# Kernel tuning notes

Hardware: AMD Instinct MI355X
Metric: run time of the kernel (lower is better)

The kernel has to match this reference:

```python
import jax, jax.numpy as jnp
import numpy as np

EPS = 1e-4
HEADS = 8
DIM_HEAD = 32
BALANCE = 0.3


def _normalize(x, dims):
    # torch normalize(): norm over `dims` in fp32; norm = eps + norm*sqrt(norm.numel()/x.numel())
    red = 1
    for d in dims:
        red *= x.shape[d]
    norm = jnp.sqrt(jnp.sum(jnp.square(x.astype(jnp.float32)), axis=dims, keepdims=True))
    norm = EPS + norm / np.sqrt(red)
    return x / norm.astype(x.dtype)


def _mpconv1x1(x, w, gain=1.0):
    # MPConv forward (eval mode): weight-normalize per output channel, scale, 1x1 conv
    w = w.astype(jnp.float32)
    w = _normalize(w, (1, 2, 3))
    fan_in = w.shape[1] * w.shape[2] * w.shape[3]
    w = (w * (gain / np.sqrt(fan_in))).astype(x.dtype)[:, :, 0, 0]  # [out, in]
    return jnp.einsum('oi,nihw->nohw', w, x)


def setup_inputs() -> dict:
    key = jax.random.key(0)
    k1, k2, k3 = jax.random.split(key, 3)
    x = jax.random.normal(k1, (2, 256, 48, 48), dtype=jnp.float32)
    w_qkv = jax.random.normal(k2, (768, 256, 1, 1), dtype=jnp.float32)
    w_out = jax.random.normal(k3, (256, 256, 1, 1), dtype=jnp.float32)
    return {"x": x, "w_qkv": w_qkv, "w_out": w_out}


def reference(x, w_qkv, w_out):
    n, c, h, w_sp = x.shape
    seq = h * w_sp
    y = _mpconv1x1(x, w_qkv)                          # [n, 3c, h, w]
    y = y.reshape(n, HEADS, DIM_HEAD, 3, seq)         # channel split: head x dim_head x 3
    y = _normalize(y, (2,))                           # L2-normalize over dim_head axis
    q = y[:, :, :, 0, :]
    k = y[:, :, :, 1, :]
    v = y[:, :, :, 2, :]
    # scores [n, h, q, k] with k scaled by 1/sqrt(dim_head)
    att = jax.nn.softmax(jnp.einsum('nhcq,nhck->nhqk', q, k) / np.sqrt(DIM_HEAD), axis=3)
    y = jnp.einsum('nhqk,nhck->nhcq', att, v)         # [n, heads, dim_head, seq]
    y = _mpconv1x1(y.reshape(n, c, h, w_sp), w_out)
    t = BALANCE
    # mp_sum: lerp then magnitude-preserving rescale
    return (x + t * (y - x)) / np.sqrt((1 - t) ** 2 + t ** 2)
```

## Files before the change

### kernel.cpp

```cpp
#include <hip/hip_runtime.h>
#include <math.h>

#define EPSN 1e-4f
#define SEQ 2304

using bf16x8 = __attribute__((ext_vector_type(8))) short;
using f32x4  = __attribute__((ext_vector_type(4))) float;

__device__ inline unsigned short f2bf(float x) {
    union { float f; unsigned u; } c; c.f = x;
    unsigned u = c.u;
    u += 0x7fffu + ((u >> 16) & 1u);
    return (unsigned short)(u >> 16);
}

__device__ inline unsigned cvt_pk_bf16(float lo, float hi) {
    unsigned r;
    asm("v_cvt_pk_bf16_f32 %0, %1, %2" : "=v"(r) : "v"(lo), "v"(hi));
    return r;
}
__device__ inline void permlane32_swap(unsigned &a, unsigned &b) {
    asm("v_permlane32_swap_b32 %0, %1" : "+v"(a), "+v"(b));
}
__device__ inline void permlane16_swap(unsigned &a, unsigned &b) {
    asm("v_permlane16_swap_b32 %0, %1" : "+v"(a), "+v"(b));
}

__global__ __launch_bounds__(256) void prep_kernel(const float* __restrict__ w_qkv,
                                                   const float* __restrict__ w_out,
                                                   const float* __restrict__ x,
                                                   unsigned short* __restrict__ wqb,
                                                   unsigned short* __restrict__ wob,
                                                   unsigned short* __restrict__ xt) {
    __shared__ __align__(16) unsigned short T[16][72];
    int bid = blockIdx.x;
    if (bid < 256) {
        int wave = threadIdx.x >> 6, lane = threadIdx.x & 63;
        int row = bid * 4 + wave;
        const float* src;
        unsigned short* dst;
        if (row < 768) { src = w_qkv + (size_t)row * 256; dst = wqb + (size_t)row * 256; }
        else           { src = w_out + (size_t)(row - 768) * 256; dst = wob + (size_t)(row - 768) * 256; }
        float4 v = *(const float4*)&src[lane * 4];
        float ss = v.x * v.x + v.y * v.y + v.z * v.z + v.w * v.w;
        for (int off = 32; off > 0; off >>= 1) ss += __shfl_xor(ss, off, 64);
        float sc = 1.0f / (sqrtf(ss) + 16.0f * EPSN);
        unsigned p0 = (unsigned)f2bf(v.x * sc) | ((unsigned)f2bf(v.y * sc) << 16);
        unsigned p1 = (unsigned)f2bf(v.z * sc) | ((unsigned)f2bf(v.w * sc) << 16);
        *(uint2*)&dst[lane * 4] = make_uint2(p0, p1);
    } else {
        int e0 = bid - 256;
        int n = e0 / 576;
        int r = e0 % 576;
        int ct = r / 144;
        int r2 = r % 144;
        int st = r2 >> 2, sq = r2 & 3;
        int tid = threadIdx.x;
        int c = tid >> 2, sv = (tid & 3) * 4;
        float4 v = *(const float4*)&x[(size_t)(n * 256 + ct * 64 + c) * SEQ + st * 64 + sq * 16 + sv];
        T[sv + 0][c] = f2bf(v.x);
        T[sv + 1][c] = f2bf(v.y);
        T[sv + 2][c] = f2bf(v.z);
        T[sv + 3][c] = f2bf(v.w);
        __syncthreads();
        int s = tid >> 4, cb = (tid & 15) * 4;
        uint2 t2 = *(const uint2*)&T[s][cb];
        *(uint2*)&xt[(size_t)(n * SEQ + st * 64 + sq * 16 + s) * 256 + ct * 64 + cb] = t2;
    }
}

__global__ __launch_bounds__(256) void qkv_fused_kernel(const unsigned short* __restrict__ xt,
                                                        const unsigned short* __restrict__ wqb,
                                                        unsigned short* __restrict__ qn,
                                                        unsigned short* __restrict__ kn,
                                                        unsigned short* __restrict__ vn) {
    __shared__ float Cs[96][65];
    __shared__ __align__(16) unsigned short Vls[32][72];
    int bid = blockIdx.x;
    int xcd = bid & 7, j = bid >> 3;
    int h = j & 7;
    int tilej = xcd * 9 + (j >> 3);
    int st = tilej % 36, n = tilej / 36;
    int tid = threadIdx.x;
    int wave = tid >> 6, lane = tid & 63;
    int ln = lane & 15, quad = lane >> 4;
    const unsigned short* Abase = wqb + (size_t)(h * 96 + ln) * 256 + quad * 8;
    const unsigned short* Bbase = xt + (size_t)(n * SEQ + st * 64 + wave * 16 + ln) * 256 + quad * 8;
    f32x4 acc[6];
#pragma unroll
    for (int m = 0; m < 6; ++m) acc[m] = (f32x4){0.f, 0.f, 0.f, 0.f};
#pragma unroll
    for (int kc = 0; kc < 8; ++kc) {
        bf16x8 b = *(const bf16x8*)(Bbase + kc * 32);
#pragma unroll
        for (int m = 0; m < 6; ++m) {
            bf16x8 a = *(const bf16x8*)(Abase + (size_t)(m * 16) * 256 + kc * 32);
            acc[m] = __builtin_amdgcn_mfma_f32_16x16x32_bf16(a, b, acc[m], 0, 0, 0);
        }
    }
#pragma unroll
    for (int m = 0; m < 6; ++m)
#pragma unroll
        for (int r = 0; r < 4; ++r)
            Cs[m * 16 + quad * 4 + r][wave * 16 + ln] = acc[m][r];
    __syncthreads();
    int nh = n * 8 + h;
    if (tid < 192) {
        int sl = tid & 63, wh = tid >> 6;
        int s = st * 64 + sl;
        float v[32];
        float ss = 0.f;
#pragma unroll
        for (int d = 0; d < 32; ++d) { v[d] = Cs[3 * d + wh][sl]; ss += v[d] * v[d]; }
        float inv = 1.0f / (EPSN + sqrtf(ss * (1.0f / 32.0f)));
        if (wh == 0) inv *= 0.17677669529663687f * 1.4426950408889634f;
        if (wh == 2) {
#pragma unroll
            for (int d = 0; d < 32; ++d) Vls[d][sl] = f2bf(v[d] * inv);
        } else {
            unsigned short* dst = (wh == 1 ? kn : qn) + (size_t)nh * 73728 + (size_t)s * 32;
            unsigned wbuf[16];
#pragma unroll
            for (int j2 = 0; j2 < 16; ++j2)
                wbuf[j2] = (unsigned)f2bf(v[2 * j2] * inv) | ((unsigned)f2bf(v[2 * j2 + 1] * inv) << 16);
#pragma unroll
            for (int j2 = 0; j2 < 4; ++j2) {
                uint4 t4 = make_uint4(wbuf[4 * j2], wbuf[4 * j2 + 1], wbuf[4 * j2 + 2], wbuf[4 * j2 + 3]);
                *(uint4*)(dst + j2 * 8) = t4;
            }
        }
    }
    __syncthreads();
    {
        int d = tid >> 3, sj = (tid & 7) * 8;
        uint4 t4 = *(const uint4*)&Vls[d][sj];
        *(uint4*)&vn[(size_t)nh * 73728 + (size_t)d * SEQ + st * 64 + sj] = t4;
    }
}

__global__ __launch_bounds__(256) void attn_mfma_kernel(const unsigned short* __restrict__ qn,
                                                        const unsigned short* __restrict__ kn,
                                                        const unsigned short* __restrict__ vn,
                                                        float* __restrict__ Opart,
                                                        float* __restrict__ Lpart) {
    __shared__ __align__(16) unsigned short Ks[2][64][40];
    __shared__ __align__(16) unsigned short Vs[2][32][72];
    int tid = threadIdx.x;
    int wq = tid >> 6, lane = tid & 63;
    int ln = lane & 15, quad = lane >> 4;
    int bid = blockIdx.x;
    int xcd = bid & 7, bi = bid >> 3;
    int nh = xcd * 2 + (bi >= 72);
    int bi2 = (bi >= 72) ? bi - 72 : bi;
    int qt = bi2 % 36, kz = bi2 / 36;
    const unsigned short* Qg = qn + (size_t)nh * 73728;
    const unsigned short* Kg = kn + (size_t)nh * 73728;
    const unsigned short* Vg = vn + (size_t)nh * 73728;

    bf16x8 qf = *(const bf16x8*)(Qg + (size_t)(qt * 64 + wq * 16 + ln) * 32 + quad * 8);
    bf16x8 ones;
#pragma unroll
    for (int i = 0; i < 8; ++i) ones[i] = (short)0x3F80;

    f32x4 o0 = {0.f, 0.f, 0.f, 0.f};
    f32x4 o1 = {0.f, 0.f, 0.f, 0.f};
    f32x4 lac = {0.f, 0.f, 0.f, 0.f};

    int s0 = kz * 18 * 64;

    auto compute_tile = [&](int bsel) {
        const f32x4 zero = {0.f, 0.f, 0.f, 0.f};
        unsigned w[4][2];
#pragma unroll
        for (int c = 0; c < 4; ++c) {
            bf16x8 kf = *(const bf16x8*)(&Ks[bsel][c * 16 + ln][quad * 8]);
            f32x4 sc = __builtin_amdgcn_mfma_f32_16x16x32_bf16(kf, qf, zero, 0, 0, 0);
            w[c][0] = cvt_pk_bf16(exp2f(sc[0]), exp2f(sc[1]));
            w[c][1] = cvt_pk_bf16(exp2f(sc[2]), exp2f(sc[3]));
        }
#pragma unroll
        for (int kc = 0; kc < 2; ++kc) {
            unsigned a0 = w[2 * kc][0], b0 = w[2 * kc + 1][0];
            permlane32_swap(a0, b0);
            permlane16_swap(a0, b0);
            unsigned a1 = w[2 * kc][1], b1 = w[2 * kc + 1][1];
            permlane32_swap(a1, b1);
            permlane16_swap(a1, b1);
            union { unsigned u[4]; bf16x8 v8; } pk;
            pk.u[0] = a0; pk.u[1] = a1; pk.u[2] = b0; pk.u[3] = b1;
            bf16x8 v0 = *(const bf16x8*)(&Vs[bsel][ln][kc * 32 + quad * 8]);
            bf16x8 v1 = *(const bf16x8*)(&Vs[bsel][16 + ln][kc * 32 + quad * 8]);
            lac = __builtin_amdgcn_mfma_f32_16x16x32_bf16(pk.v8, ones, lac, 0, 0, 0);
            o0  = __builtin_amdgcn_mfma_f32_16x16x32_bf16(pk.v8, v0, o0, 0, 0, 0);
            o1  = __builtin_amdgcn_mfma_f32_16x16x32_bf16(pk.v8, v1, o1, 0, 0, 0);
        }
    };

    uint4 kA = *(const uint4*)(Kg + (size_t)s0 * 32 + tid * 8);
    uint4 vA = *(const uint4*)(Vg + (size_t)(tid >> 3) * SEQ + s0 + (tid & 7) * 8);
    *(uint4*)(&Ks[0][tid >> 2][(tid & 3) * 8]) = kA;
    *(uint4*)(&Vs[0][tid >> 3][(tid & 7) * 8]) = vA;
    uint4 kB = *(const uint4*)(Kg + (size_t)(s0 + 64) * 32 + tid * 8);
    uint4 vB = *(const uint4*)(Vg + (size_t)(tid >> 3) * SEQ + (s0 + 64) + (tid & 7) * 8);

    for (int i = 0; i < 18; i += 2) {
        if (i + 2 < 18) {
            int sn = s0 + (i + 2) * 64;
            kA = *(const uint4*)(Kg + (size_t)sn * 32 + tid * 8);
            vA = *(const uint4*)(Vg + (size_t)(tid >> 3) * SEQ + sn + (tid & 7) * 8);
        }
        __syncthreads();
        compute_tile(0);
        *(uint4*)(&Ks[1][tid >> 2][(tid & 3) * 8]) = kB;
        *(uint4*)(&Vs[1][tid >> 3][(tid & 7) * 8]) = vB;
        if (i + 3 < 18) {
            int sn = s0 + (i + 3) * 64;
            kB = *(const uint4*)(Kg + (size_t)sn * 32 + tid * 8);
            vB = *(const uint4*)(Vg + (size_t)(tid >> 3) * SEQ + sn + (tid & 7) * 8);
        }
        __syncthreads();
        compute_tile(1);
        if (i + 2 < 18) {
            *(uint4*)(&Ks[0][tid >> 2][(tid & 3) * 8]) = kA;
            *(uint4*)(&Vs[0][tid >> 3][(tid & 7) * 8]) = vA;
        }
    }

    float* Ob = Opart + ((size_t)(kz * 16 + nh) * 36 + qt) * 2048;
    float* Lb = Lpart + ((size_t)(kz * 16 + nh) * 36 + qt) * 64;
#pragma unroll
    for (int r = 0; r < 4; ++r) {
        int ql = wq * 16 + quad * 4 + r;
        Ob[ql * 32 + ln]      = o0[r];
        Ob[ql * 32 + 16 + ln] = o1[r];
        if (ln == 0) Lb[ql] = lac[r];
    }
}

__global__ __launch_bounds__(256) void attn_reduce_kernel(const float* __restrict__ Opart,
                                                          const float* __restrict__ Lpart,
                                                          unsigned short* __restrict__ y2t) {
    int qt = blockIdx.x, nh = blockIdx.y;
    int n = nh >> 3, h = nh & 7;
    size_t s0 = (size_t)nh * 36 + qt;
    const float* O0 = Opart + s0 * 2048;
    const float* O1 = Opart + (s0 + 16 * 36) * 2048;
    const float* L0 = Lpart + s0 * 64;
    const float* L1 = Lpart + (s0 + 16 * 36) * 64;
#pragma unroll
    for (int p = 0; p < 2; ++p) {
        int idx = (threadIdx.x + p * 256) * 4;
        int q = idx >> 5, c = idx & 31;
        float inv = 1.0f / (L0[q] + L1[q]);
        float4 a = *(const float4*)&O0[idx];
        float4 b = *(const float4*)&O1[idx];
        float r0 = (a.x + b.x) * inv;
        float r1 = (a.y + b.y) * inv;
        float r2 = (a.z + b.z) * inv;
        float r3 = (a.w + b.w) * inv;
        *(uint2*)&y2t[((size_t)(n * SEQ) + qt * 64 + q) * 256 + h * 32 + c] =
            make_uint2(cvt_pk_bf16(r0, r1), cvt_pk_bf16(r2, r3));
    }
}

__global__ __launch_bounds__(256) void out_gemm_kernel(const unsigned short* __restrict__ y2t,
                                                       const unsigned short* __restrict__ wob,
                                                       const float* __restrict__ x,
                                                       float* __restrict__ out) {
    int st = blockIdx.x;
    int mt = blockIdx.y;
    int n  = blockIdx.z;
    int tid = threadIdx.x;
    int wave = tid >> 6, lane = tid & 63;
    int ln = lane & 15, quad = lane >> 4;
    int m0 = mt * 64 + wave * 16;
    const unsigned short* Abase = wob + (size_t)(m0 + ln) * 256 + quad * 8;
    const unsigned short* Bbase = y2t + (size_t)(n * SEQ + st * 32 + ln) * 256 + quad * 8;
    f32x4 acc[2];
#pragma unroll
    for (int c = 0; c < 2; ++c) acc[c] = (f32x4){0.f, 0.f, 0.f, 0.f};
#pragma unroll
    for (int kc = 0; kc < 8; ++kc) {
        bf16x8 a = *(const bf16x8*)(Abase + kc * 32);
#pragma unroll
        for (int c = 0; c < 2; ++c) {
            bf16x8 b = *(const bf16x8*)(Bbase + (size_t)(c * 16) * 256 + kc * 32);
            acc[c] = __builtin_amdgcn_mfma_f32_16x16x32_bf16(a, b, acc[c], 0, 0, 0);
        }
    }
    const float c0f = 0.7f * 1.3130643285972254f;
    const float c1f = 0.3f * 1.3130643285972254f;
#pragma unroll
    for (int c = 0; c < 2; ++c)
#pragma unroll
        for (int r = 0; r < 4; ++r) {
            int o = m0 + quad * 4 + r;
            int s = st * 32 + c * 16 + ln;
            size_t idx = (size_t)(n * 256 + o) * SEQ + s;
            out[idx] = c0f * x[idx] + c1f * acc[c][r];
        }
}

extern "C" void kernel_launch(void* const* d_in, const int* in_sizes, int n_in,
                              void* d_out, int out_size, void* d_ws, size_t ws_size,
                              hipStream_t stream) {
    (void)in_sizes; (void)n_in; (void)out_size; (void)ws_size;
    const float* x     = (const float*)d_in[0];
    const float* w_qkv = (const float*)d_in[1];
    const float* w_out = (const float*)d_in[2];
    float* out = (float*)d_out;
    float* ws  = (float*)d_ws;
    unsigned short* wqb = (unsigned short*)(ws);
    unsigned short* wob = (unsigned short*)(ws + 98304);
    unsigned short* xt  = (unsigned short*)(ws + 131072);
    unsigned short* y2t = (unsigned short*)(ws + 131072);
    unsigned short* qn  = (unsigned short*)(ws + 720896);
    unsigned short* kn  = (unsigned short*)(ws + 1310720);
    unsigned short* vn  = (unsigned short*)(ws + 1900544);
    float* Opart = ws + 2490368;
    float* Lpart = ws + 4849664;

    hipLaunchKernelGGL(prep_kernel, dim3(1408), dim3(256), 0, stream,
                       w_qkv, w_out, x, wqb, wob, xt);
    hipLaunchKernelGGL(qkv_fused_kernel, dim3(576), dim3(256), 0, stream,
                       xt, wqb, qn, kn, vn);
    hipLaunchKernelGGL(attn_mfma_kernel, dim3(1152), dim3(256), 0, stream,
                       qn, kn, vn, Opart, Lpart);
    hipLaunchKernelGGL(attn_reduce_kernel, dim3(36, 16), dim3(256), 0, stream,
                       Opart, Lpart, y2t);
    hipLaunchKernelGGL(out_gemm_kernel, dim3(72, 4, 2), dim3(256), 0, stream,
                       y2t, wob, x, out);
}
```

Baseline: 134.7 us.

## Double grid sizes: finer QKV/out tiles and 4-way key split in attention

```diff
diff --git a/kernel.cpp b/kernel.cpp
--- a/kernel.cpp
+++ b/kernel.cpp
@@ -74,40 +74,41 @@
                                                         unsigned short* __restrict__ qn,
                                                         unsigned short* __restrict__ kn,
                                                         unsigned short* __restrict__ vn) {
-    __shared__ float Cs[96][65];
-    __shared__ __align__(16) unsigned short Vls[32][72];
+    __shared__ float Cs[96][33];
+    __shared__ __align__(16) unsigned short Vls[32][40];
     int bid = blockIdx.x;
     int xcd = bid & 7, j = bid >> 3;
     int h = j & 7;
-    int tilej = xcd * 9 + (j >> 3);
-    int st = tilej % 36, n = tilej / 36;
+    int tile = xcd * 18 + (j >> 3);
+    int st2 = tile % 72, n = tile / 72;
     int tid = threadIdx.x;
     int wave = tid >> 6, lane = tid & 63;
     int ln = lane & 15, quad = lane >> 4;
-    const unsigned short* Abase = wqb + (size_t)(h * 96 + ln) * 256 + quad * 8;
-    const unsigned short* Bbase = xt + (size_t)(n * SEQ + st * 64 + wave * 16 + ln) * 256 + quad * 8;
-    f32x4 acc[6];
-#pragma unroll
-    for (int m = 0; m < 6; ++m) acc[m] = (f32x4){0.f, 0.f, 0.f, 0.f};
+    int sgrp = wave & 1, mgrp = wave >> 1;
+    const unsigned short* Abase = wqb + (size_t)(h * 96 + mgrp * 48 + ln) * 256 + quad * 8;
+    const unsigned short* Bbase = xt + (size_t)(n * SEQ + st2 * 32 + sgrp * 16 + ln) * 256 + quad * 8;
+    f32x4 acc[3];
+#pragma unroll
+    for (int m = 0; m < 3; ++m) acc[m] = (f32x4){0.f, 0.f, 0.f, 0.f};
 #pragma unroll
     for (int kc = 0; kc < 8; ++kc) {
         bf16x8 b = *(const bf16x8*)(Bbase + kc * 32);
 #pragma unroll
-        for (int m = 0; m < 6; ++m) {
+        for (int m = 0; m < 3; ++m) {
             bf16x8 a = *(const bf16x8*)(Abase + (size_t)(m * 16) * 256 + kc * 32);
             acc[m] = __builtin_amdgcn_mfma_f32_16x16x32_bf16(a, b, acc[m], 0, 0, 0);
         }
     }
 #pragma unroll
-    for (int m = 0; m < 6; ++m)
+    for (int m = 0; m < 3; ++m)
 #pragma unroll
         for (int r = 0; r < 4; ++r)
-            Cs[m * 16 + quad * 4 + r][wave * 16 + ln] = acc[m][r];
+            Cs[mgrp * 48 + m * 16 + quad * 4 + r][sgrp * 16 + ln] = acc[m][r];
     __syncthreads();
     int nh = n * 8 + h;
-    if (tid < 192) {
-        int sl = tid & 63, wh = tid >> 6;
-        int s = st * 64 + sl;
+    if (tid < 96) {
+        int sl = tid & 31, wh = tid >> 5;
+        int s = st2 * 32 + sl;
         float v[32];
         float ss = 0.f;
 #pragma unroll
@@ -132,9 +133,9 @@
     }
     __syncthreads();
     {
-        int d = tid >> 3, sj = (tid & 7) * 8;
-        uint4 t4 = *(const uint4*)&Vls[d][sj];
-        *(uint4*)&vn[(size_t)nh * 73728 + (size_t)d * SEQ + st * 64 + sj] = t4;
+        int d = tid >> 3, sj = (tid & 7) * 4;
+        uint2 t2 = *(const uint2*)&Vls[d][sj];
+        *(uint2*)&vn[(size_t)nh * 73728 + (size_t)d * SEQ + st2 * 32 + sj] = t2;
     }
 }
 
@@ -150,8 +151,8 @@
     int ln = lane & 15, quad = lane >> 4;
     int bid = blockIdx.x;
     int xcd = bid & 7, bi = bid >> 3;
-    int nh = xcd * 2 + (bi >= 72);
-    int bi2 = (bi >= 72) ? bi - 72 : bi;
+    int nh = xcd * 2 + (bi >= 144);
+    int bi2 = (bi >= 144) ? bi - 144 : bi;
     int qt = bi2 % 36, kz = bi2 / 36;
     const unsigned short* Qg = qn + (size_t)nh * 73728;
     const unsigned short* Kg = kn + (size_t)nh * 73728;
@@ -166,7 +167,8 @@
     f32x4 o1 = {0.f, 0.f, 0.f, 0.f};
     f32x4 lac = {0.f, 0.f, 0.f, 0.f};
 
-    int s0 = kz * 18 * 64;
+    const int NT = 9;
+    int s0 = kz * NT * 64;
 
     auto compute_tile = [&](int bsel) {
         const f32x4 zero = {0.f, 0.f, 0.f, 0.f};
@@ -203,24 +205,26 @@
     uint4 kB = *(const uint4*)(Kg + (size_t)(s0 + 64) * 32 + tid * 8);
     uint4 vB = *(const uint4*)(Vg + (size_t)(tid >> 3) * SEQ + (s0 + 64) + (tid & 7) * 8);
 
-    for (int i = 0; i < 18; i += 2) {
-        if (i + 2 < 18) {
+    for (int i = 0; i < NT; i += 2) {
+        if (i + 2 < NT) {
             int sn = s0 + (i + 2) * 64;
             kA = *(const uint4*)(Kg + (size_t)sn * 32 + tid * 8);
             vA = *(const uint4*)(Vg + (size_t)(tid >> 3) * SEQ + sn + (tid & 7) * 8);
         }
         __syncthreads();
         compute_tile(0);
-        *(uint4*)(&Ks[1][tid >> 2][(tid & 3) * 8]) = kB;
-        *(uint4*)(&Vs[1][tid >> 3][(tid & 7) * 8]) = vB;
-        if (i + 3 < 18) {
+        if (i + 1 < NT) {
+            *(uint4*)(&Ks[1][tid >> 2][(tid & 3) * 8]) = kB;
+            *(uint4*)(&Vs[1][tid >> 3][(tid & 7) * 8]) = vB;
+        }
+        if (i + 3 < NT) {
             int sn = s0 + (i + 3) * 64;
             kB = *(const uint4*)(Kg + (size_t)sn * 32 + tid * 8);
             vB = *(const uint4*)(Vg + (size_t)(tid >> 3) * SEQ + sn + (tid & 7) * 8);
         }
         __syncthreads();
-        compute_tile(1);
-        if (i + 2 < 18) {
+        if (i + 1 < NT) compute_tile(1);
+        if (i + 2 < NT) {
             *(uint4*)(&Ks[0][tid >> 2][(tid & 3) * 8]) = kA;
             *(uint4*)(&Vs[0][tid >> 3][(tid & 7) * 8]) = vA;
         }
@@ -244,20 +248,26 @@
     int n = nh >> 3, h = nh & 7;
     size_t s0 = (size_t)nh * 36 + qt;
     const float* O0 = Opart + s0 * 2048;
-    const float* O1 = Opart + (s0 + 16 * 36) * 2048;
+    const float* O1 = Opart + (s0 + 1 * 576) * 2048;
+    const float* O2 = Opart + (s0 + 2 * 576) * 2048;
+    const float* O3 = Opart + (s0 + 3 * 576) * 2048;
     const float* L0 = Lpart + s0 * 64;
-    const float* L1 = Lpart + (s0 + 16 * 36) * 64;
+    const float* L1 = Lpart + (s0 + 1 * 576) * 64;
+    const float* L2 = Lpart + (s0 + 2 * 576) * 64;
+    const float* L3 = Lpart + (s0 + 3 * 576) * 64;
 #pragma unroll
     for (int p = 0; p < 2; ++p) {
         int idx = (threadIdx.x + p * 256) * 4;
         int q = idx >> 5, c = idx & 31;
-        float inv = 1.0f / (L0[q] + L1[q]);
+        float inv = 1.0f / (L0[q] + L1[q] + L2[q] + L3[q]);
         float4 a = *(const float4*)&O0[idx];
         float4 b = *(const float4*)&O1[idx];
-        float r0 = (a.x + b.x) * inv;
-        float r1 = (a.y + b.y) * inv;
-        float r2 = (a.z + b.z) * inv;
-        float r3 = (a.w + b.w) * inv;
+        float4 e = *(const float4*)&O2[idx];
+        float4 f = *(const float4*)&O3[idx];
+        float r0 = ((a.x + b.x) + (e.x + f.x)) * inv;
+        float r1 = ((a.y + b.y) + (e.y + f.y)) * inv;
+        float r2 = ((a.z + b.z) + (e.z + f.z)) * inv;
+        float r3 = ((a.w + b.w) + (e.w + f.w)) * inv;
         *(uint2*)&y2t[((size_t)(n * SEQ) + qt * 64 + q) * 256 + h * 32 + c] =
             make_uint2(cvt_pk_bf16(r0, r1), cvt_pk_bf16(r2, r3));
     }
@@ -267,38 +277,34 @@
                                                        const unsigned short* __restrict__ wob,
                                                        const float* __restrict__ x,
                                                        float* __restrict__ out) {
-    int st = blockIdx.x;
-    int mt = blockIdx.y;
-    int n  = blockIdx.z;
+    int bid = blockIdx.x;
+    int xcd = bid & 7, j = bid >> 3;
+    int mt = j & 3;
+    int u = j >> 2;
+    int n = u & 1;
+    int st = xcd * 18 + (u >> 1);
     int tid = threadIdx.x;
     int wave = tid >> 6, lane = tid & 63;
     int ln = lane & 15, quad = lane >> 4;
     int m0 = mt * 64 + wave * 16;
     const unsigned short* Abase = wob + (size_t)(m0 + ln) * 256 + quad * 8;
-    const unsigned short* Bbase = y2t + (size_t)(n * SEQ + st * 32 + ln) * 256 + quad * 8;
-    f32x4 acc[2];
-#pragma unroll
-    for (int c = 0; c < 2; ++c) acc[c] = (f32x4){0.f, 0.f, 0.f, 0.f};
+    const unsigned short* Bbase = y2t + (size_t)(n * SEQ + st * 16 + ln) * 256 + quad * 8;
+    f32x4 acc = (f32x4){0.f, 0.f, 0.f, 0.f};
 #pragma unroll
     for (int kc = 0; kc < 8; ++kc) {
         bf16x8 a = *(const bf16x8*)(Abase + kc * 32);
-#pragma unroll
-        for (int c = 0; c < 2; ++c) {
-            bf16x8 b = *(const bf16x8*)(Bbase + (size_t)(c * 16) * 256 + kc * 32);
-            acc[c] = __builtin_amdgcn_mfma_f32_16x16x32_bf16(a, b, acc[c], 0, 0, 0);
-        }
+        bf16x8 b = *(const bf16x8*)(Bbase + kc * 32);
+        acc = __builtin_amdgcn_mfma_f32_16x16x32_bf16(a, b, acc, 0, 0, 0);
     }
     const float c0f = 0.7f * 1.3130643285972254f;
     const float c1f = 0.3f * 1.3130643285972254f;
 #pragma unroll
-    for (int c = 0; c < 2; ++c)
-#pragma unroll
-        for (int r = 0; r < 4; ++r) {
-            int o = m0 + quad * 4 + r;
-            int s = st * 32 + c * 16 + ln;
-            size_t idx = (size_t)(n * 256 + o) * SEQ + s;
-            out[idx] = c0f * x[idx] + c1f * acc[c][r];
-        }
+    for (int r = 0; r < 4; ++r) {
+        int o = m0 + quad * 4 + r;
+        int s = st * 16 + ln;
+        size_t idx = (size_t)(n * 256 + o) * SEQ + s;
+        out[idx] = c0f * x[idx] + c1f * acc[r];
+    }
 }
 
 extern "C" void kernel_launch(void* const* d_in, const int* in_sizes, int n_in,
@@ -318,16 +324,16 @@
     unsigned short* kn  = (unsigned short*)(ws + 1310720);
     unsigned short* vn  = (unsigned short*)(ws + 1900544);
     float* Opart = ws + 2490368;
-    float* Lpart = ws + 4849664;
+    float* Lpart = ws + 7208960;
 
     hipLaunchKernelGGL(prep_kernel, dim3(1408), dim3(256), 0, stream,
                        w_qkv, w_out, x, wqb, wob, xt);
-    hipLaunchKernelGGL(qkv_fused_kernel, dim3(576), dim3(256), 0, stream,
+    hipLaunchKernelGGL(qkv_fused_kernel, dim3(1152), dim3(256), 0, stream,
                        xt, wqb, qn, kn, vn);
-    hipLaunchKernelGGL(attn_mfma_kernel, dim3(1152), dim3(256), 0, stream,
+    hipLaunchKernelGGL(attn_mfma_kernel, dim3(2304), dim3(256), 0, stream,
                        qn, kn, vn, Opart, Lpart);
     hipLaunchKernelGGL(attn_reduce_kernel, dim3(36, 16), dim3(256), 0, stream,
                        Opart, Lpart, y2t);
-    hipLaunchKernelGGL(out_gemm_kernel, dim3(72, 4, 2), dim3(256), 0, stream,
+    hipLaunchKernelGGL(out_gemm_kernel, dim3(1152), dim3(256), 0, stream,
                        y2t, wob, x, out);
 }
```

Result: faster. 129.9 us (-3.5%).
